# Performance work log

Hardware: AMD Instinct MI355X
Metric: run time of the kernel (lower is better)

## Reference

```python
import jax, jax.numpy as jnp
import numpy as np

N = 40000; E = 640000; F_IN = 128; HID = 32; HEADS = 4; G = 64
NEG_SLOPE = 0.2; LN_EPS = 1e-5


def setup_inputs() -> dict:
    key = jax.random.key(0)
    ks = jax.random.split(key, 24)
    rn = lambda k, shape, s=0.1: jax.random.normal(k, shape, jnp.float32) * s
    d = {}
    d["x"] = jax.random.normal(ks[0], (N, F_IN), jnp.float32)
    d["edge_index"] = jax.random.randint(ks[1], (2, E), 0, N)
    d["batch"] = jnp.sort(jax.random.randint(ks[2], (N,), 0, G))
    # GAT layer 0: in F_IN -> HID per head, HEADS heads, concat
    d["W0"] = rn(ks[3], (F_IN, HEADS * HID))
    d["as0"] = rn(ks[4], (HEADS, HID)); d["ad0"] = rn(ks[5], (HEADS, HID))
    d["b0"] = jnp.zeros((HEADS * HID,), jnp.float32)
    d["ln0_g"] = jnp.ones((HEADS * HID,), jnp.float32); d["ln0_b"] = jnp.zeros((HEADS * HID,), jnp.float32)
    # GAT layer 1: HEADS*HID -> HID per head, HEADS heads, concat
    d["W1"] = rn(ks[6], (HEADS * HID, HEADS * HID))
    d["as1"] = rn(ks[7], (HEADS, HID)); d["ad1"] = rn(ks[8], (HEADS, HID))
    d["b1"] = jnp.zeros((HEADS * HID,), jnp.float32)
    d["ln1_g"] = jnp.ones((HEADS * HID,), jnp.float32); d["ln1_b"] = jnp.zeros((HEADS * HID,), jnp.float32)
    # GAT layer 2: HEADS*HID -> HID, 1 head, no concat
    d["W2"] = rn(ks[9], (HEADS * HID, HID))
    d["as2"] = rn(ks[10], (1, HID)); d["ad2"] = rn(ks[11], (1, HID))
    d["b2"] = jnp.zeros((HID,), jnp.float32)
    d["ln2_g"] = jnp.ones((HID,), jnp.float32); d["ln2_b"] = jnp.zeros((HID,), jnp.float32)
    # classifier: HID -> HID//2 -> 2
    d["fc1_w"] = rn(ks[12], (HID, HID // 2)); d["fc1_b"] = jnp.zeros((HID // 2,), jnp.float32)
    d["fc2_w"] = rn(ks[13], (HID // 2, 2)); d["fc2_b"] = jnp.zeros((2,), jnp.float32)
    return d


def gat_layer(x, src, dst, W, a_s, a_d, b, heads, out_c, concat):
    n = x.shape[0]
    h = (x @ W).reshape(n, heads, out_c)            # [N,H,C]
    al_s = jnp.sum(h * a_s, axis=-1)                # [N,H]
    al_d = jnp.sum(h * a_d, axis=-1)                # [N,H]
    e = jax.nn.leaky_relu(al_s[src] + al_d[dst], NEG_SLOPE)  # [E,H]
    m = jax.ops.segment_max(e, dst, num_segments=n)          # segment softmax over dst
    ex = jnp.exp(e - m[dst])
    s = jax.ops.segment_sum(ex, dst, num_segments=n)
    alpha = ex / (s[dst] + 1e-16)                   # [E,H]
    out = jax.ops.segment_sum(h[src] * alpha[:, :, None], dst, num_segments=n)  # [N,H,C]
    out = out.reshape(n, heads * out_c) if concat else out.mean(axis=1)
    return out + b


def layer_norm(x, g, b):
    mu = x.mean(-1, keepdims=True)
    var = jnp.var(x, axis=-1, keepdims=True)
    return (x - mu) * jax.lax.rsqrt(var + LN_EPS) * g + b


def reference(x, edge_index, batch, W0, as0, ad0, b0, ln0_g, ln0_b, W1, as1, ad1, b1, ln1_g, ln1_b, W2, as2, ad2, b2, ln2_g, ln2_b, fc1_w, fc1_b, fc2_w, fc2_b):
    src, dst = edge_index[0], edge_index[1]
    h = gat_layer(x, src, dst, W0, as0, ad0, b0, HEADS, HID, True)
    h = jax.nn.elu(layer_norm(h, ln0_g, ln0_b))
    h = gat_layer(h, src, dst, W1, as1, ad1, b1, HEADS, HID, True)
    h = jax.nn.elu(layer_norm(h, ln1_g, ln1_b))
    h = gat_layer(h, src, dst, W2, as2, ad2, b2, 1, HID, False)
    h = jax.nn.elu(layer_norm(h, ln2_g, ln2_b))
    cnt = jax.ops.segment_sum(jnp.ones((h.shape[0],), h.dtype), batch, num_segments=G)
    hg = jax.ops.segment_sum(h, batch, num_segments=G) / jnp.maximum(cnt, 1.0)[:, None]  # global mean pool [G,HID]
    z = jax.nn.relu(hg @ fc1_w + fc1_b)
    return z @ fc2_w + fc2_b
```

## Files before the change

### kernel.cpp

```cpp
#include <hip/hip_runtime.h>
#include <hip/hip_fp16.h>
#include <math.h>

#define NN 40000
#define EE 640000
#define NG 64
#define SCAN_BLOCKS ((NN + 1023) / 1024)

__device__ __forceinline__ float eluf(float x) { return x > 0.f ? x : expm1f(x); }

typedef const __attribute__((address_space(1))) char gas_char;
typedef __attribute__((address_space(3))) char las_char;

__device__ __forceinline__ void async_copy16(void* l, const void* g) {
  __builtin_amdgcn_global_load_lds((gas_char*)g, (las_char*)l, 16, 0, 0);
}

typedef __fp16 f16x2 __attribute__((ext_vector_type(2)));
__device__ __forceinline__ unsigned packh(float lo, float hi) {
  f16x2 p = __builtin_amdgcn_cvt_pkrtz(lo, hi);
  union { f16x2 h; unsigned u; } c; c.h = p; return c.u;
}
__device__ __forceinline__ float hlo(unsigned p) {
  union { unsigned u; f16x2 h; } c; c.u = p; return (float)c.h.x;
}
__device__ __forceinline__ float hhi(unsigned p) {
  union { unsigned u; f16x2 h; } c; c.u = p; return (float)c.h.y;
}

__global__ void zero_int_kernel(int* __restrict__ p, int n) {
  int i = blockIdx.x * 256 + threadIdx.x;
  if (i < n) p[i] = 0;
}

__global__ void count_deg_kernel(const int* __restrict__ dst, int* __restrict__ deg, int e) {
  int i = blockIdx.x * 256 + threadIdx.x;
  if (i < e) atomicAdd(&deg[dst[i]], 1);
}

__global__ __launch_bounds__(1024) void scanA_kernel(const int* __restrict__ deg,
                                                     int* __restrict__ row_ptr,
                                                     int* __restrict__ bsum, int n) {
  __shared__ int wsum[16];
  int t = threadIdx.x, lane = t & 63, wid = t >> 6;
  int i = blockIdx.x * 1024 + t;
  int v = (i < n) ? deg[i] : 0;
#pragma unroll
  for (int off = 1; off < 64; off <<= 1) {
    int u = __shfl_up(v, off);
    if (lane >= off) v += u;
  }
  if (lane == 63) wsum[wid] = v;
  __syncthreads();
  if (t < 16) {
    int w = wsum[t];
#pragma unroll
    for (int off = 1; off < 16; off <<= 1) {
      int u = __shfl_up(w, off);
      if (t >= off) w += u;
    }
    wsum[t] = w;
  }
  __syncthreads();
  if (wid > 0) v += wsum[wid - 1];
  if (i < n) row_ptr[i + 1] = v;
  if (t == 1023) bsum[blockIdx.x] = v;
}

__global__ __launch_bounds__(1024) void scanC_kernel(int* __restrict__ row_ptr,
                                                     const int* __restrict__ bsum,
                                                     int* __restrict__ cursor, int n) {
  __shared__ int off_s;
  int t = threadIdx.x;
  int b = blockIdx.x;
  if (t < 64) {
    int v = (t < b && t < SCAN_BLOCKS) ? bsum[t] : 0;
#pragma unroll
    for (int m = 1; m < 64; m <<= 1) v += __shfl_xor(v, m);
    if (t == 0) off_s = v;
  }
  __syncthreads();
  int off = off_s;
  int i = b * 1024 + t;
  if (i < n) {
    int v = row_ptr[i + 1] + off;
    row_ptr[i + 1] = v;
    if (i + 1 < n) cursor[i + 1] = v;
    if (i == 0) { cursor[0] = 0; row_ptr[0] = 0; }
  }
}

__global__ void scatter_kernel(const int* __restrict__ src, const int* __restrict__ dst,
                               int* __restrict__ cursor, int* __restrict__ csr_src, int e) {
  int i = blockIdx.x * 256 + threadIdx.x;
  if (i < e) {
    int d = dst[i];
    int pos = atomicAdd(&cursor[d], 1);
    csr_src[pos] = src[i];
  }
}

__global__ __launch_bounds__(256, 3) void gemm128_kernel(
    const float* __restrict__ x, const float* __restrict__ W,
    const float* __restrict__ a_s, const float* __restrict__ a_d,
    unsigned* __restrict__ hb, float* __restrict__ als, float* __restrict__ ald)
{
  __shared__ float xs[2][64 * 32];
  __shared__ float ws[2][32 * 128];

  int t = threadIdx.x;
  int row0 = blockIdx.x * 64;
  const char* xgb = (const char*)x + (size_t)row0 * 512;

  {
    int li0 = t, li1 = t + 256;
    async_copy16((char*)xs[0] + li0 * 16, xgb + (li0 >> 3) * 512 + (li0 & 7) * 16);
    async_copy16((char*)xs[0] + li1 * 16, xgb + (li1 >> 3) * 512 + (li1 & 7) * 16);
    const char* wg = (const char*)W;
#pragma unroll
    for (int p = 0; p < 4; ++p)
      async_copy16((char*)ws[0] + p * 4096 + t * 16, wg + p * 4096 + t * 16);
  }
  __syncthreads();

  int cg = t & 31, rg = t >> 5;
  int r0 = rg * 8;
  int jlo = 2 * cg;

  float acc[8][4];
#pragma unroll
  for (int r = 0; r < 8; ++r)
#pragma unroll
    for (int c = 0; c < 4; ++c) acc[r][c] = 0.f;

  for (int ch = 0; ch < 4; ++ch) {
    if (ch < 3) {
      int b = (ch + 1) & 1;
      int li0 = t, li1 = t + 256;
      const char* xg = xgb + (ch + 1) * 128;
      async_copy16((char*)xs[b] + li0 * 16, xg + (li0 >> 3) * 512 + (li0 & 7) * 16);
      async_copy16((char*)xs[b] + li1 * 16, xg + (li1 >> 3) * 512 + (li1 & 7) * 16);
      const char* wg = (const char*)W + (size_t)(ch + 1) * 32 * 128 * 4;
#pragma unroll
      for (int p = 0; p < 4; ++p)
        async_copy16((char*)ws[b] + p * 4096 + t * 16, wg + p * 4096 + t * 16);
    }
    const float* wc = ws[ch & 1];
    const float* xc = xs[ch & 1];
#pragma unroll
    for (int kk = 0; kk < 32; kk += 4) {
      float2 wlo[4], whi[4];
#pragma unroll
      for (int q = 0; q < 4; ++q) {
        wlo[q] = *reinterpret_cast<const float2*>(&wc[(kk + q) * 128 + jlo]);
        whi[q] = *reinterpret_cast<const float2*>(&wc[(kk + q) * 128 + 64 + jlo]);
      }
#pragma unroll
      for (int r = 0; r < 8; ++r) {
        float4 xv = *reinterpret_cast<const float4*>(&xc[(r0 + r) * 32 + kk]);
        float a0 = acc[r][0], a1 = acc[r][1], a2 = acc[r][2], a3 = acc[r][3];
        a0 = fmaf(xv.x, wlo[0].x, a0); a1 = fmaf(xv.x, wlo[0].y, a1);
        a2 = fmaf(xv.x, whi[0].x, a2); a3 = fmaf(xv.x, whi[0].y, a3);
        a0 = fmaf(xv.y, wlo[1].x, a0); a1 = fmaf(xv.y, wlo[1].y, a1);
        a2 = fmaf(xv.y, whi[1].x, a2); a3 = fmaf(xv.y, whi[1].y, a3);
        a0 = fmaf(xv.z, wlo[2].x, a0); a1 = fmaf(xv.z, wlo[2].y, a1);
        a2 = fmaf(xv.z, whi[2].x, a2); a3 = fmaf(xv.z, whi[2].y, a3);
        a0 = fmaf(xv.w, wlo[3].x, a0); a1 = fmaf(xv.w, wlo[3].y, a1);
        a2 = fmaf(xv.w, whi[3].x, a2); a3 = fmaf(xv.w, whi[3].y, a3);
        acc[r][0] = a0; acc[r][1] = a1; acc[r][2] = a2; acc[r][3] = a3;
      }
    }
    __syncthreads();
  }

#pragma unroll
  for (int r = 0; r < 8; ++r) {
    uint2 pv;
    pv.x = packh(acc[r][0], acc[r][2]);
    pv.y = packh(acc[r][1], acc[r][3]);
    *reinterpret_cast<uint2*>(&hb[(size_t)(row0 + r0 + r) * 64 + jlo]) = pv;
  }

  float as0 = a_s[jlo], as1 = a_s[jlo + 1], as2 = a_s[jlo + 64], as3 = a_s[jlo + 65];
  float ad0 = a_d[jlo], ad1 = a_d[jlo + 1], ad2 = a_d[jlo + 64], ad3 = a_d[jlo + 65];
  int lane = t & 63;
#pragma unroll
  for (int r = 0; r < 8; ++r) {
    float psa = fmaf(acc[r][0], as0, acc[r][1] * as1);
    float psb = fmaf(acc[r][2], as2, acc[r][3] * as3);
    float pda = fmaf(acc[r][0], ad0, acc[r][1] * ad1);
    float pdb = fmaf(acc[r][2], ad2, acc[r][3] * ad3);
#pragma unroll
    for (int m = 1; m < 16; m <<= 1) {
      psa += __shfl_xor(psa, m); psb += __shfl_xor(psb, m);
      pda += __shfl_xor(pda, m); pdb += __shfl_xor(pdb, m);
    }
    if ((lane & 15) == 0) {
      int hA = (lane >> 4) & 1;
      size_t row = (size_t)(row0 + r0 + r);
      als[row * 4 + hA] = psa; als[row * 4 + hA + 2] = psb;
      ald[row * 4 + hA] = pda; ald[row * 4 + hA + 2] = pdb;
    }
  }
}

__global__ __launch_bounds__(256, 2) void gemm32_kernel(
    const float* __restrict__ x, const float* __restrict__ W,
    const float* __restrict__ a_s, const float* __restrict__ a_d,
    float* __restrict__ h, float* __restrict__ als, float* __restrict__ ald)
{
  __shared__ float xs[64 * 128];
  __shared__ float ws[2][32 * 32];
  int t = threadIdx.x;
  int row0 = blockIdx.x * 64;
  {
    const char* xg = (const char*)(x + (size_t)row0 * 128);
    char* xl = (char*)xs;
#pragma unroll
    for (int it = 0; it < 8; ++it)
      async_copy16(xl + it * 4096 + t * 16, xg + it * 4096 + t * 16);
  }
  async_copy16((char*)ws[0] + t * 16, (const char*)W + t * 16);
  __syncthreads();

  int cg = t & 7, rg = t >> 3;
  int r0 = rg * 2, c0 = cg * 4;
  float acc[2][4];
#pragma unroll
  for (int r = 0; r < 2; ++r)
#pragma unroll
    for (int c = 0; c < 4; ++c) acc[r][c] = 0.f;

  for (int ch = 0; ch < 4; ++ch) {
    if (ch < 3) {
      const char* wg = (const char*)W + (size_t)(ch + 1) * 32 * 32 * 4;
      async_copy16((char*)ws[(ch + 1) & 1] + t * 16, wg + t * 16);
    }
    const float* wc = ws[ch & 1];
    const float* xc = xs + ch * 32;
#pragma unroll
    for (int kk = 0; kk < 32; kk += 4) {
      float4 wv[4];
#pragma unroll
      for (int q = 0; q < 4; ++q)
        wv[q] = *reinterpret_cast<const float4*>(&wc[(kk + q) * 32 + c0]);
#pragma unroll
      for (int r = 0; r < 2; ++r) {
        float4 xv = *reinterpret_cast<const float4*>(&xc[(r0 + r) * 128 + kk]);
#pragma unroll
        for (int c = 0; c < 4; ++c) {
          float a = acc[r][c];
          a = fmaf(xv.x, (&wv[0].x)[c], a);
          a = fmaf(xv.y, (&wv[1].x)[c], a);
          a = fmaf(xv.z, (&wv[2].x)[c], a);
          a = fmaf(xv.w, (&wv[3].x)[c], a);
          acc[r][c] = a;
        }
      }
    }
    __syncthreads();
  }

#pragma unroll
  for (int r = 0; r < 2; ++r) {
    float4 hv = make_float4(acc[r][0], acc[r][1], acc[r][2], acc[r][3]);
    *reinterpret_cast<float4*>(&h[(size_t)(row0 + r0 + r) * 32 + c0]) = hv;
  }
  float asv[4], adv[4];
#pragma unroll
  for (int c = 0; c < 4; ++c) { asv[c] = a_s[c0 + c]; adv[c] = a_d[c0 + c]; }
#pragma unroll
  for (int r = 0; r < 2; ++r) {
    float ps = acc[r][0] * asv[0] + acc[r][1] * asv[1] + acc[r][2] * asv[2] + acc[r][3] * asv[3];
    float pd = acc[r][0] * adv[0] + acc[r][1] * adv[1] + acc[r][2] * adv[2] + acc[r][3] * adv[3];
#pragma unroll
    for (int m = 1; m < 8; m <<= 1) { ps += __shfl_xor(ps, m); pd += __shfl_xor(pd, m); }
    if ((t & 7) == 0) {
      als[row0 + r0 + r] = ps;
      ald[row0 + r0 + r] = pd;
    }
  }
}

__global__ __launch_bounds__(256) void aggregate128_kernel(
    const unsigned* __restrict__ hb, const float* __restrict__ als, const float* __restrict__ ald,
    const int* __restrict__ row_ptr, const int* __restrict__ csr_src,
    const float* __restrict__ bias, const float* __restrict__ ln_g, const float* __restrict__ ln_b,
    float* __restrict__ out, int n)
{
  __shared__ int s_src[4][2][32];
  __shared__ float2 s_w[4][2][32][2];
  int t = threadIdx.x, lane = t & 63, wid = t >> 6;
  int hw = lane >> 5, c = lane & 31;
  int node = blockIdx.x * 8 + wid * 2 + hw;
  int start = row_ptr[node], end = row_ptr[node + 1];
  int deg = end - start;

  float4 adq = reinterpret_cast<const float4*>(ald)[node];
  int hsel = c >> 4;
  float a0 = 0.f, a1 = 0.f, a2 = 0.f, a3 = 0.f;
  float ssum0 = 0.f, ssum1 = 0.f;

  if (deg <= 32) {
    int s = 0;
    float ex0 = 0.f, ex1 = 0.f, ex2 = 0.f, ex3 = 0.f;
    if (c < deg) {
      s = csr_src[start + c];
      float4 q = reinterpret_cast<const float4*>(als)[s];
      float v0 = q.x + adq.x, v1 = q.y + adq.y, v2 = q.z + adq.z, v3 = q.w + adq.w;
      v0 = v0 > 0.f ? v0 : 0.2f * v0; v1 = v1 > 0.f ? v1 : 0.2f * v1;
      v2 = v2 > 0.f ? v2 : 0.2f * v2; v3 = v3 > 0.f ? v3 : 0.2f * v3;
      ex0 = __expf(v0); ex1 = __expf(v1); ex2 = __expf(v2); ex3 = __expf(v3);
    }
    s_src[wid][hw][c] = s;
    s_w[wid][hw][c][0] = make_float2(ex0, ex2);
    s_w[wid][hw][c][1] = make_float2(ex1, ex3);

    float b0a = 0.f, b1a = 0.f, b2a = 0.f, b3a = 0.f;
    float sb0 = 0.f, sb1 = 0.f;
    int j = 0;
    for (; j + 2 <= deg; j += 2) {
      int sa = s_src[wid][hw][j];
      int sb = s_src[wid][hw][j + 1];
      uint2 ua = *reinterpret_cast<const uint2*>(&hb[(size_t)sa * 64 + 2 * c]);
      uint2 ub = *reinterpret_cast<const uint2*>(&hb[(size_t)sb * 64 + 2 * c]);
      float2 wa = s_w[wid][hw][j][hsel];
      float2 wb = s_w[wid][hw][j + 1][hsel];
      a0 = fmaf(wa.x, hlo(ua.x), a0); a1 = fmaf(wa.x, hlo(ua.y), a1);
      a2 = fmaf(wa.y, hhi(ua.x), a2); a3 = fmaf(wa.y, hhi(ua.y), a3);
      ssum0 += wa.x; ssum1 += wa.y;
      b0a = fmaf(wb.x, hlo(ub.x), b0a); b1a = fmaf(wb.x, hlo(ub.y), b1a);
      b2a = fmaf(wb.y, hhi(ub.x), b2a); b3a = fmaf(wb.y, hhi(ub.y), b3a);
      sb0 += wb.x; sb1 += wb.y;
    }
    if (j < deg) {
      int sa = s_src[wid][hw][j];
      uint2 ua = *reinterpret_cast<const uint2*>(&hb[(size_t)sa * 64 + 2 * c]);
      float2 wa = s_w[wid][hw][j][hsel];
      a0 = fmaf(wa.x, hlo(ua.x), a0); a1 = fmaf(wa.x, hlo(ua.y), a1);
      a2 = fmaf(wa.y, hhi(ua.x), a2); a3 = fmaf(wa.y, hhi(ua.y), a3);
      ssum0 += wa.x; ssum1 += wa.y;
    }
    a0 += b0a; a1 += b1a; a2 += b2a; a3 += b3a;
    ssum0 += sb0; ssum1 += sb1;
  } else {
    for (int eb = 0; eb < deg; eb += 32) {
      int s = 0;
      float ex0 = 0.f, ex1 = 0.f, ex2 = 0.f, ex3 = 0.f;
      if (eb + c < deg) {
        s = csr_src[start + eb + c];
        float4 q = reinterpret_cast<const float4*>(als)[s];
        float v0 = q.x + adq.x, v1 = q.y + adq.y, v2 = q.z + adq.z, v3 = q.w + adq.w;
        v0 = v0 > 0.f ? v0 : 0.2f * v0; v1 = v1 > 0.f ? v1 : 0.2f * v1;
        v2 = v2 > 0.f ? v2 : 0.2f * v2; v3 = v3 > 0.f ? v3 : 0.2f * v3;
        ex0 = __expf(v0); ex1 = __expf(v1); ex2 = __expf(v2); ex3 = __expf(v3);
      }
      s_src[wid][hw][c] = s;
      s_w[wid][hw][c][0] = make_float2(ex0, ex2);
      s_w[wid][hw][c][1] = make_float2(ex1, ex3);
      int cnt = deg - eb; if (cnt > 32) cnt = 32;
      for (int j = 0; j < cnt; ++j) {
        int sj = s_src[wid][hw][j];
        uint2 u = *reinterpret_cast<const uint2*>(&hb[(size_t)sj * 64 + 2 * c]);
        float2 w = s_w[wid][hw][j][hsel];
        a0 = fmaf(w.x, hlo(u.x), a0); a1 = fmaf(w.x, hlo(u.y), a1);
        a2 = fmaf(w.y, hhi(u.x), a2); a3 = fmaf(w.y, hhi(u.y), a3);
        ssum0 += w.x; ssum1 += w.y;
      }
    }
  }

  float2 blo = *reinterpret_cast<const float2*>(&bias[2 * c]);
  float2 bhi = *reinterpret_cast<const float2*>(&bias[2 * c + 64]);
  float is0 = 1.f / (ssum0 + 1e-16f), is1 = 1.f / (ssum1 + 1e-16f);
  float o0 = a0 * is0 + blo.x;
  float o1 = a1 * is0 + blo.y;
  float o2 = a2 * is1 + bhi.x;
  float o3 = a3 * is1 + bhi.y;
  float red = o0 + o1 + o2 + o3;
  float sq2 = o0 * o0 + o1 * o1 + o2 * o2 + o3 * o3;
#pragma unroll
  for (int m = 1; m < 32; m <<= 1) {
    red += __shfl_xor(red, m);
    sq2 += __shfl_xor(sq2, m);
  }
  float mu = red * (1.f / 128.f);
  float var = sq2 * (1.f / 128.f) - mu * mu;
  float rstd = rsqrtf(var + 1e-5f);
  float2 glo = *reinterpret_cast<const float2*>(&ln_g[2 * c]);
  float2 ghi = *reinterpret_cast<const float2*>(&ln_g[2 * c + 64]);
  float2 bl2 = *reinterpret_cast<const float2*>(&ln_b[2 * c]);
  float2 bh2 = *reinterpret_cast<const float2*>(&ln_b[2 * c + 64]);
  float2 ylo, yhi;
  ylo.x = eluf((o0 - mu) * rstd * glo.x + bl2.x);
  ylo.y = eluf((o1 - mu) * rstd * glo.y + bl2.y);
  yhi.x = eluf((o2 - mu) * rstd * ghi.x + bh2.x);
  yhi.y = eluf((o3 - mu) * rstd * ghi.y + bh2.y);
  *reinterpret_cast<float2*>(&out[(size_t)node * 128 + 2 * c]) = ylo;
  *reinterpret_cast<float2*>(&out[(size_t)node * 128 + 64 + 2 * c]) = yhi;
}

__global__ __launch_bounds__(256) void aggregate32_kernel(
    const float* __restrict__ h, const float* __restrict__ als, const float* __restrict__ ald,
    const int* __restrict__ row_ptr, const int* __restrict__ csr_src,
    const float* __restrict__ bias, const float* __restrict__ ln_g, const float* __restrict__ ln_b,
    float* __restrict__ out, int n)
{
  __shared__ int s_src[4][2][32];
  __shared__ float s_ex[4][2][32];
  int t = threadIdx.x, lane = t & 63, wid = t >> 6;
  int hw = lane >> 5, c = lane & 31;
  int node = blockIdx.x * 8 + wid * 2 + hw;
  int start = row_ptr[node], end = row_ptr[node + 1];
  int deg = end - start;
  float adl = ald[node];
  float acc0 = 0.f, ssum = 0.f;

  if (deg <= 32) {
    int s = 0; float ex = 0.f;
    if (c < deg) {
      s = csr_src[start + c];
      float v = als[s] + adl;
      v = v > 0.f ? v : 0.2f * v;
      ex = __expf(v);
    }
    s_src[wid][hw][c] = s;
    s_ex[wid][hw][c] = ex;

    float acc1 = 0.f, ssum1 = 0.f;
    int j = 0;
    for (; j + 2 <= deg; j += 2) {
      int sa = s_src[wid][hw][j];
      int sb = s_src[wid][hw][j + 1];
      float ha = h[(size_t)sa * 32 + c];
      float hbv = h[(size_t)sb * 32 + c];
      float wa = s_ex[wid][hw][j];
      float wb = s_ex[wid][hw][j + 1];
      acc0 = fmaf(wa, ha, acc0); ssum += wa;
      acc1 = fmaf(wb, hbv, acc1); ssum1 += wb;
    }
    if (j < deg) {
      float wa = s_ex[wid][hw][j];
      acc0 = fmaf(wa, h[(size_t)s_src[wid][hw][j] * 32 + c], acc0);
      ssum += wa;
    }
    acc0 += acc1; ssum += ssum1;
  } else {
    for (int eb = 0; eb < deg; eb += 32) {
      int s = 0; float ex = 0.f;
      if (eb + c < deg) {
        s = csr_src[start + eb + c];
        float v = als[s] + adl;
        v = v > 0.f ? v : 0.2f * v;
        ex = __expf(v);
      }
      s_src[wid][hw][c] = s;
      s_ex[wid][hw][c] = ex;
      int cnt = deg - eb; if (cnt > 32) cnt = 32;
      for (int j = 0; j < cnt; ++j) {
        float w = s_ex[wid][hw][j];
        acc0 = fmaf(w, h[(size_t)s_src[wid][hw][j] * 32 + c], acc0);
        ssum += w;
      }
    }
  }

  float o0 = acc0 / (ssum + 1e-16f) + bias[c];
  float red = o0, sq2 = o0 * o0;
#pragma unroll
  for (int m = 1; m < 32; m <<= 1) {
    red += __shfl_xor(red, m);
    sq2 += __shfl_xor(sq2, m);
  }
  float mu = red * (1.f / 32.f);
  float var = sq2 * (1.f / 32.f) - mu * mu;
  float rstd = rsqrtf(var + 1e-5f);
  float y0 = (o0 - mu) * rstd * ln_g[c] + ln_b[c];
  out[(size_t)node * 32 + c] = eluf(y0);
}

__device__ __forceinline__ int lower_bound_dev(const int* a, int n, int key) {
  int lo = 0, hi = n;
  while (lo < hi) { int mid = (lo + hi) >> 1; if (a[mid] < key) lo = mid + 1; else hi = mid; }
  return lo;
}

__global__ __launch_bounds__(256) void poolfc_kernel(
    const float* __restrict__ x2, const int* __restrict__ batch,
    const float* __restrict__ fc1w, const float* __restrict__ fc1b,
    const float* __restrict__ fc2w, const float* __restrict__ fc2b,
    float* __restrict__ out, int n)
{
  int g = blockIdx.x;
  int lo = lower_bound_dev(batch, n, g);
  int hi = lower_bound_dev(batch, n, g + 1);
  int t = threadIdx.x;
  int c = t & 31, r = t >> 5;
  float acc = 0.f;
  for (int i = lo + r; i < hi; i += 8) acc += x2[(size_t)i * 32 + c];
  __shared__ float red[8][32];
  __shared__ float hgl[32];
  __shared__ float zl[16];
  red[r][c] = acc;
  __syncthreads();
  if (r == 0) {
    float s = 0.f;
#pragma unroll
    for (int k = 0; k < 8; ++k) s += red[k][c];
    float cnt = (float)(hi - lo);
    hgl[c] = s / fmaxf(cnt, 1.f);
  }
  __syncthreads();
  if (t < 16) {
    float a = fc1b[t];
#pragma unroll
    for (int k = 0; k < 32; ++k) a = fmaf(hgl[k], fc1w[k * 16 + t], a);
    zl[t] = fmaxf(a, 0.f);
  }
  __syncthreads();
  if (t < 2) {
    float a = fc2b[t];
#pragma unroll
    for (int j = 0; j < 16; ++j) a = fmaf(zl[j], fc2w[j * 2 + t], a);
    out[g * 2 + t] = a;
  }
}

extern "C" void kernel_launch(void* const* d_in, const int* in_sizes, int n_in,
                              void* d_out, int out_size, void* d_ws, size_t ws_size,
                              hipStream_t stream) {
  const float* x    = (const float*)d_in[0];
  const int*   ei   = (const int*)d_in[1];
  const int*   batch= (const int*)d_in[2];
  const float* W0   = (const float*)d_in[3];
  const float* as0  = (const float*)d_in[4];
  const float* ad0  = (const float*)d_in[5];
  const float* b0   = (const float*)d_in[6];
  const float* ln0g = (const float*)d_in[7];
  const float* ln0b = (const float*)d_in[8];
  const float* W1   = (const float*)d_in[9];
  const float* as1  = (const float*)d_in[10];
  const float* ad1  = (const float*)d_in[11];
  const float* b1   = (const float*)d_in[12];
  const float* ln1g = (const float*)d_in[13];
  const float* ln1b = (const float*)d_in[14];
  const float* W2   = (const float*)d_in[15];
  const float* as2  = (const float*)d_in[16];
  const float* ad2  = (const float*)d_in[17];
  const float* b2   = (const float*)d_in[18];
  const float* ln2g = (const float*)d_in[19];
  const float* ln2b = (const float*)d_in[20];
  const float* fc1w = (const float*)d_in[21];
  const float* fc1b = (const float*)d_in[22];
  const float* fc2w = (const float*)d_in[23];
  const float* fc2b = (const float*)d_in[24];
  float* out = (float*)d_out;

  const int* srce = ei;
  const int* dste = ei + EE;

  unsigned* hb = (unsigned*)d_ws;
  float* B2  = (float*)(hb + (size_t)NN * 64);
  float* als = B2 + (size_t)NN * 128;
  float* ald = als + (size_t)NN * 4;
  float* h2  = ald + (size_t)NN * 4;
  float* x2  = h2 + (size_t)NN * 32;
  int* deg      = (int*)(x2 + (size_t)NN * 32);
  int* row_ptr  = deg + NN;
  int* cursor   = row_ptr + NN + 1;
  int* csr_src  = cursor + NN;
  int* bsum     = csr_src + EE;

  zero_int_kernel<<<(NN + 255) / 256, 256, 0, stream>>>(deg, NN);
  count_deg_kernel<<<(EE + 255) / 256, 256, 0, stream>>>(dste, deg, EE);
  scanA_kernel<<<SCAN_BLOCKS, 1024, 0, stream>>>(deg, row_ptr, bsum, NN);
  scanC_kernel<<<SCAN_BLOCKS, 1024, 0, stream>>>(row_ptr, bsum, cursor, NN);
  scatter_kernel<<<(EE + 255) / 256, 256, 0, stream>>>(srce, dste, cursor, csr_src, EE);

  gemm128_kernel<<<625, 256, 0, stream>>>(x, W0, as0, ad0, hb, als, ald);
  aggregate128_kernel<<<NN / 8, 256, 0, stream>>>(hb, als, ald, row_ptr, csr_src,
                                                  b0, ln0g, ln0b, B2, NN);
  gemm128_kernel<<<625, 256, 0, stream>>>(B2, W1, as1, ad1, hb, als, ald);
  aggregate128_kernel<<<NN / 8, 256, 0, stream>>>(hb, als, ald, row_ptr, csr_src,
                                                  b1, ln1g, ln1b, B2, NN);
  gemm32_kernel<<<625, 256, 0, stream>>>(B2, W2, as2, ad2, h2, als, ald);
  aggregate32_kernel<<<NN / 8, 256, 0, stream>>>(h2, als, ald, row_ptr, csr_src,
                                                 b2, ln2g, ln2b, x2, NN);
  poolfc_kernel<<<NG, 256, 0, stream>>>(x2, batch, fc1w, fc1b, fc2w, fc2b, out, NN);
}
```

Baseline: 255.1 us.

## Fuse layer-2 linear projection into layer-1 aggregation epilogue, store fp16 features

Removes the separate gemm32 kernel. Layer-1 aggregation now stages the normalized 128-wide row in shared memory and multiplies it by a transposed W2 held in LDS, producing the 32-wide projection and attention logits in the same pass. The projected features are stored as fp16, which halves gather traffic in the final aggregation. This avoids writing and re-reading the 40000x128 intermediate, at the cost of extra LDS (about 17KB per block), a W2 load in every block, and reduced precision in layer-2 features.

```diff
diff --git a/kernel.cpp b/kernel.cpp
--- a/kernel.cpp
+++ b/kernel.cpp
@@ -26,6 +26,9 @@
 }
 __device__ __forceinline__ float hhi(unsigned p) {
   union { unsigned u; f16x2 h; } c; c.u = p; return (float)c.h.y;
+}
+__device__ __forceinline__ float h16f(unsigned short u) {
+  union { unsigned u32; f16x2 h; } c; c.u32 = u; return (float)c.h.x;
 }
 
 __global__ void zero_int_kernel(int* __restrict__ p, int n) {
@@ -204,95 +207,33 @@
   }
 }
 
-__global__ __launch_bounds__(256, 2) void gemm32_kernel(
-    const float* __restrict__ x, const float* __restrict__ W,
-    const float* __restrict__ a_s, const float* __restrict__ a_d,
-    float* __restrict__ h, float* __restrict__ als, float* __restrict__ ald)
-{
-  __shared__ float xs[64 * 128];
-  __shared__ float ws[2][32 * 32];
-  int t = threadIdx.x;
-  int row0 = blockIdx.x * 64;
-  {
-    const char* xg = (const char*)(x + (size_t)row0 * 128);
-    char* xl = (char*)xs;
-#pragma unroll
-    for (int it = 0; it < 8; ++it)
-      async_copy16(xl + it * 4096 + t * 16, xg + it * 4096 + t * 16);
-  }
-  async_copy16((char*)ws[0] + t * 16, (const char*)W + t * 16);
-  __syncthreads();
-
-  int cg = t & 7, rg = t >> 3;
-  int r0 = rg * 2, c0 = cg * 4;
-  float acc[2][4];
-#pragma unroll
-  for (int r = 0; r < 2; ++r)
-#pragma unroll
-    for (int c = 0; c < 4; ++c) acc[r][c] = 0.f;
-
-  for (int ch = 0; ch < 4; ++ch) {
-    if (ch < 3) {
-      const char* wg = (const char*)W + (size_t)(ch + 1) * 32 * 32 * 4;
-      async_copy16((char*)ws[(ch + 1) & 1] + t * 16, wg + t * 16);
-    }
-    const float* wc = ws[ch & 1];
-    const float* xc = xs + ch * 32;
-#pragma unroll
-    for (int kk = 0; kk < 32; kk += 4) {
-      float4 wv[4];
-#pragma unroll
-      for (int q = 0; q < 4; ++q)
-        wv[q] = *reinterpret_cast<const float4*>(&wc[(kk + q) * 32 + c0]);
-#pragma unroll
-      for (int r = 0; r < 2; ++r) {
-        float4 xv = *reinterpret_cast<const float4*>(&xc[(r0 + r) * 128 + kk]);
-#pragma unroll
-        for (int c = 0; c < 4; ++c) {
-          float a = acc[r][c];
-          a = fmaf(xv.x, (&wv[0].x)[c], a);
-          a = fmaf(xv.y, (&wv[1].x)[c], a);
-          a = fmaf(xv.z, (&wv[2].x)[c], a);
-          a = fmaf(xv.w, (&wv[3].x)[c], a);
-          acc[r][c] = a;
-        }
-      }
-    }
-    __syncthreads();
-  }
-
-#pragma unroll
-  for (int r = 0; r < 2; ++r) {
-    float4 hv = make_float4(acc[r][0], acc[r][1], acc[r][2], acc[r][3]);
-    *reinterpret_cast<float4*>(&h[(size_t)(row0 + r0 + r) * 32 + c0]) = hv;
-  }
-  float asv[4], adv[4];
-#pragma unroll
-  for (int c = 0; c < 4; ++c) { asv[c] = a_s[c0 + c]; adv[c] = a_d[c0 + c]; }
-#pragma unroll
-  for (int r = 0; r < 2; ++r) {
-    float ps = acc[r][0] * asv[0] + acc[r][1] * asv[1] + acc[r][2] * asv[2] + acc[r][3] * asv[3];
-    float pd = acc[r][0] * adv[0] + acc[r][1] * adv[1] + acc[r][2] * adv[2] + acc[r][3] * adv[3];
-#pragma unroll
-    for (int m = 1; m < 8; m <<= 1) { ps += __shfl_xor(ps, m); pd += __shfl_xor(pd, m); }
-    if ((t & 7) == 0) {
-      als[row0 + r0 + r] = ps;
-      ald[row0 + r0 + r] = pd;
-    }
-  }
-}
-
+template<bool FUSE>
 __global__ __launch_bounds__(256) void aggregate128_kernel(
     const unsigned* __restrict__ hb, const float* __restrict__ als, const float* __restrict__ ald,
     const int* __restrict__ row_ptr, const int* __restrict__ csr_src,
     const float* __restrict__ bias, const float* __restrict__ ln_g, const float* __restrict__ ln_b,
-    float* __restrict__ out, int n)
+    float* __restrict__ out,
+    const float* __restrict__ W2, const float* __restrict__ as2, const float* __restrict__ ad2,
+    unsigned short* __restrict__ h2h, float* __restrict__ als2, float* __restrict__ ald2)
 {
   __shared__ int s_src[4][2][32];
   __shared__ float2 s_w[4][2][32][2];
+  __shared__ __align__(16) float w2t[FUSE ? 32 * 132 : 4];
+  __shared__ __align__(16) float y_s[FUSE ? 8 * 128 : 4];
+
   int t = threadIdx.x, lane = t & 63, wid = t >> 6;
   int hw = lane >> 5, c = lane & 31;
   int node = blockIdx.x * 8 + wid * 2 + hw;
+
+  if constexpr (FUSE) {
+#pragma unroll
+    for (int i = 0; i < 16; ++i) {
+      int e = i * 256 + t;
+      w2t[(e & 31) * 132 + (e >> 5)] = W2[e];
+    }
+    __syncthreads();
+  }
+
   int start = row_ptr[node], end = row_ptr[node + 1];
   int deg = end - start;
 
@@ -396,12 +337,33 @@
   ylo.y = eluf((o1 - mu) * rstd * glo.y + bl2.y);
   yhi.x = eluf((o2 - mu) * rstd * ghi.x + bh2.x);
   yhi.y = eluf((o3 - mu) * rstd * ghi.y + bh2.y);
-  *reinterpret_cast<float2*>(&out[(size_t)node * 128 + 2 * c]) = ylo;
-  *reinterpret_cast<float2*>(&out[(size_t)node * 128 + 64 + 2 * c]) = yhi;
+
+  if constexpr (!FUSE) {
+    *reinterpret_cast<float2*>(&out[(size_t)node * 128 + 2 * c]) = ylo;
+    *reinterpret_cast<float2*>(&out[(size_t)node * 128 + 64 + 2 * c]) = yhi;
+  } else {
+    int nidx = (wid * 2 + hw) * 128;
+    *reinterpret_cast<float2*>(&y_s[nidx + 2 * c]) = ylo;
+    *reinterpret_cast<float2*>(&y_s[nidx + 64 + 2 * c]) = yhi;
+    float acc = 0.f;
+    const float* wrow = &w2t[c * 132];
+#pragma unroll
+    for (int k = 0; k < 128; k += 4) {
+      float4 yv = *reinterpret_cast<const float4*>(&y_s[nidx + k]);
+      float4 wv = *reinterpret_cast<const float4*>(&wrow[k]);
+      acc = fmaf(yv.x, wv.x, acc); acc = fmaf(yv.y, wv.y, acc);
+      acc = fmaf(yv.z, wv.z, acc); acc = fmaf(yv.w, wv.w, acc);
+    }
+    h2h[(size_t)node * 32 + c] = (unsigned short)(packh(acc, acc) & 0xffffu);
+    float ps = acc * as2[c], pd = acc * ad2[c];
+#pragma unroll
+    for (int m = 1; m < 32; m <<= 1) { ps += __shfl_xor(ps, m); pd += __shfl_xor(pd, m); }
+    if (c == 0) { als2[node] = ps; ald2[node] = pd; }
+  }
 }
 
 __global__ __launch_bounds__(256) void aggregate32_kernel(
-    const float* __restrict__ h, const float* __restrict__ als, const float* __restrict__ ald,
+    const unsigned short* __restrict__ h, const float* __restrict__ als, const float* __restrict__ ald,
     const int* __restrict__ row_ptr, const int* __restrict__ csr_src,
     const float* __restrict__ bias, const float* __restrict__ ln_g, const float* __restrict__ ln_b,
     float* __restrict__ out, int n)
@@ -432,8 +394,8 @@
     for (; j + 2 <= deg; j += 2) {
       int sa = s_src[wid][hw][j];
       int sb = s_src[wid][hw][j + 1];
-      float ha = h[(size_t)sa * 32 + c];
-      float hbv = h[(size_t)sb * 32 + c];
+      float ha = h16f(h[(size_t)sa * 32 + c]);
+      float hbv = h16f(h[(size_t)sb * 32 + c]);
       float wa = s_ex[wid][hw][j];
       float wb = s_ex[wid][hw][j + 1];
       acc0 = fmaf(wa, ha, acc0); ssum += wa;
@@ -441,7 +403,7 @@
     }
     if (j < deg) {
       float wa = s_ex[wid][hw][j];
-      acc0 = fmaf(wa, h[(size_t)s_src[wid][hw][j] * 32 + c], acc0);
+      acc0 = fmaf(wa, h16f(h[(size_t)s_src[wid][hw][j] * 32 + c]), acc0);
       ssum += wa;
     }
     acc0 += acc1; ssum += ssum1;
@@ -459,7 +421,7 @@
       int cnt = deg - eb; if (cnt > 32) cnt = 32;
       for (int j = 0; j < cnt; ++j) {
         float w = s_ex[wid][hw][j];
-        acc0 = fmaf(w, h[(size_t)s_src[wid][hw][j] * 32 + c], acc0);
+        acc0 = fmaf(w, h16f(h[(size_t)s_src[wid][hw][j] * 32 + c]), acc0);
         ssum += w;
       }
     }
@@ -563,9 +525,11 @@
   float* B2  = (float*)(hb + (size_t)NN * 64);
   float* als = B2 + (size_t)NN * 128;
   float* ald = als + (size_t)NN * 4;
-  float* h2  = ald + (size_t)NN * 4;
-  float* x2  = h2 + (size_t)NN * 32;
-  int* deg      = (int*)(x2 + (size_t)NN * 32);
+  unsigned short* h2h = (unsigned short*)(ald + (size_t)NN * 4);
+  float* x2  = (float*)(h2h + (size_t)NN * 32);
+  float* als2 = x2 + (size_t)NN * 32;
+  float* ald2 = als2 + NN;
+  int* deg      = (int*)(ald2 + NN);
   int* row_ptr  = deg + NN;
   int* cursor   = row_ptr + NN + 1;
   int* csr_src  = cursor + NN;
@@ -578,13 +542,15 @@
   scatter_kernel<<<(EE + 255) / 256, 256, 0, stream>>>(srce, dste, cursor, csr_src, EE);
 
   gemm128_kernel<<<625, 256, 0, stream>>>(x, W0, as0, ad0, hb, als, ald);
-  aggregate128_kernel<<<NN / 8, 256, 0, stream>>>(hb, als, ald, row_ptr, csr_src,
-                                                  b0, ln0g, ln0b, B2, NN);
+  aggregate128_kernel<false><<<NN / 8, 256, 0, stream>>>(hb, als, ald, row_ptr, csr_src,
+                                                         b0, ln0g, ln0b, B2,
+                                                         nullptr, nullptr, nullptr,
+                                                         nullptr, nullptr, nullptr);
   gemm128_kernel<<<625, 256, 0, stream>>>(B2, W1, as1, ad1, hb, als, ald);
-  aggregate128_kernel<<<NN / 8, 256, 0, stream>>>(hb, als, ald, row_ptr, csr_src,
-                                                  b1, ln1g, ln1b, B2, NN);
-  gemm32_kernel<<<625, 256, 0, stream>>>(B2, W2, as2, ad2, h2, als, ald);
-  aggregate32_kernel<<<NN / 8, 256, 0, stream>>>(h2, als, ald, row_ptr, csr_src,
+  aggregate128_kernel<true><<<NN / 8, 256, 0, stream>>>(hb, als, ald, row_ptr, csr_src,
+                                                        b1, ln1g, ln1b, nullptr,
+                                                        W2, as2, ad2, h2h, als2, ald2);
+  aggregate32_kernel<<<NN / 8, 256, 0, stream>>>(h2h, als2, ald2, row_ptr, csr_src,
                                                  b2, ln2g, ln2b, x2, NN);
   poolfc_kernel<<<NG, 256, 0, stream>>>(x2, batch, fc1w, fc1b, fc2w, fc2b, out, NN);
 }
```

After: 256.6 us. No clear change (+0.6%).
